# Optimization experiments

Hardware: AMD Instinct MI355X
Metric: run time of the kernel (lower is better)

## Reference

```python
import jax, jax.numpy as jnp
import numpy as np


def _gcn_conv(x, edge_index, W, b):
    # PyG GCNConv: h = x @ W; out = D^{-1/2}(A+I)D^{-1/2} h + b
    N = x.shape[0]
    src, dst = edge_index[0], edge_index[1]
    # degree with self-loops (edge weights = 1)
    deg = jax.ops.segment_sum(jnp.ones(src.shape[0], x.dtype), dst, num_segments=N) + 1.0
    dis = jax.lax.rsqrt(deg)  # deg >= 1 so finite
    h = x @ W  # [N, F_out]
    norm = dis[src] * dis[dst]  # [E]
    msg = h[src] * norm[:, None]  # [E, F_out] -- dominant memory traffic
    agg = jax.ops.segment_sum(msg, dst, num_segments=N)
    # self-loop contribution: norm_ii = dis_i^2
    out = agg + h * (dis * dis)[:, None] + b
    return out


def setup_inputs() -> dict:
    key = jax.random.key(0)
    k1, k2, k3, k4, k5, k6 = jax.random.split(key, 6)
    N, E = 100000, 1600000
    in_ch, hid, out_ch = 256, 128, 64  # hid = 2*out_channels
    x = jax.random.normal(k1, (N, in_ch), dtype=jnp.float32)
    edge_index = jax.random.randint(k2, (2, E), 0, N, dtype=jnp.int64)
    # Glorot-style init for GCN weights, zero bias (PyG default)
    W1 = jax.random.normal(k3, (in_ch, hid), dtype=jnp.float32) / np.sqrt(in_ch)
    b1 = jnp.zeros((hid,), jnp.float32)
    W2 = jax.random.normal(k4, (hid, out_ch), dtype=jnp.float32) / np.sqrt(hid)
    b2 = jnp.zeros((out_ch,), jnp.float32)
    return {"x": x, "edge_index": edge_index, "W1": W1, "b1": b1, "W2": W2, "b2": b2}


def reference(x, edge_index, W1, b1, W2, b2):
    # Encoder.forward: k=2 layers of activation(GCNConv(x, edge_index))
    h = jax.nn.relu(_gcn_conv(x, edge_index, W1, b1))
    h = jax.nn.relu(_gcn_conv(h, edge_index, W2, b2))
    return h
```

## Files before the change

kernel.cpp:

```cpp
#include <hip/hip_runtime.h>
#include <math.h>

#define THREADS 256

static inline int cdiv(long long a, long long b) { return (int)((a + b - 1) / b); }

typedef __attribute__((ext_vector_type(8))) short bf16x8;
typedef __attribute__((ext_vector_type(4))) float f32x4;

__device__ inline unsigned f2bf_rne_u(float f) {
    unsigned u = __builtin_bit_cast(unsigned, f);
    return (u + 0x7FFFu + ((u >> 16) & 1u)) >> 16;
}
__device__ inline float bfu2f(unsigned h) {
    unsigned u = h << 16;
    return __builtin_bit_cast(float, u);
}


__device__ __forceinline__ void hist_body(const int* __restrict__ dst, int* __restrict__ deg,
                                          int* __restrict__ rank, int E, int blk) {
    int base = (blk * THREADS + (int)threadIdx.x) * 4;
    if (base + 3 < E) {
        int4 d = *(const int4*)(dst + base);
        int4 r;
        r.x = atomicAdd(&deg[d.x], 1);
        r.y = atomicAdd(&deg[d.y], 1);
        r.z = atomicAdd(&deg[d.z], 1);
        r.w = atomicAdd(&deg[d.w], 1);
        *(int4*)(rank + base) = r;
    } else {
        for (int e = base; e < E; ++e) rank[e] = atomicAdd(&deg[dst[e]], 1);
    }
}

__device__ __forceinline__ void bfrag_unit(const float* __restrict__ W, short* __restrict__ frag,
                                           int NCT, int ctks, int lane) {
    int Nn = NCT * 16;
    int ct = ctks % NCT;
    int ks = ctks / NCT;
    int colc = ct * 16 + (lane & 15);
    int kbase = ks * 32 + (lane >> 4) * 8;
    short* base = frag + (size_t)ctks * 1024 + lane * 8;
    #pragma unroll
    for (int j = 0; j < 8; ++j) {
        float v = W[(size_t)(kbase + j) * Nn + colc];
        unsigned h = f2bf_rne_u(v);
        base[j] = (short)h;
        base[512 + j] = (short)f2bf_rne_u(v - bfu2f(h));
    }
}

__device__ __forceinline__ void fill_body(const int* __restrict__ src, const int* __restrict__ dst,
                                          const int* __restrict__ rank, const int* __restrict__ rowptr,
                                          int* __restrict__ col, int E, int blk) {
    int base = (blk * THREADS + (int)threadIdx.x) * 4;
    if (base + 3 < E) {
        int4 d = *(const int4*)(dst + base);
        int4 r = *(const int4*)(rank + base);
        int4 s = *(const int4*)(src + base);
        col[rowptr[d.x] + r.x] = s.x;
        col[rowptr[d.y] + r.y] = s.y;
        col[rowptr[d.z] + r.z] = s.z;
        col[rowptr[d.w] + r.w] = s.w;
    } else {
        for (int e = base; e < E; ++e)
            col[rowptr[dst[e]] + rank[e]] = src[e];
    }
}

template<int NCT, int KS>
__device__ __forceinline__ void gemm_body(const float* __restrict__ A, const short* __restrict__ Bfrag,
                                          unsigned short* __restrict__ G, const float* __restrict__ dis,
                                          int M, int blk) {
    constexpr int K = KS * 32;
    constexpr int Nn = NCT * 16;
    const int lane = threadIdx.x & 63;
    const int wave = threadIdx.x >> 6;
    const int rowBase = blk * 128 + wave * 32;
    const int arow0 = rowBase + (lane & 15);
    const int kgrp = (lane >> 4) * 8;

    f32x4 acc[2][NCT] = {};

    for (int ks = 0; ks < KS; ++ks) {
        const int kbase = ks * 32 + kgrp;
        bf16x8 ahi[2], alo[2];
        #pragma unroll
        for (int t = 0; t < 2; ++t) {
            int r = arow0 + t * 16;
            if (r >= M) r = M - 1;
            const float* ap = A + (size_t)r * K + kbase;
            float4 v0 = *(const float4*)ap;
            float4 v1 = *(const float4*)(ap + 4);
            float av[8] = {v0.x, v0.y, v0.z, v0.w, v1.x, v1.y, v1.z, v1.w};
            #pragma unroll
            for (int j = 0; j < 8; ++j) {
                unsigned h = f2bf_rne_u(av[j]);
                ahi[t][j] = (short)h;
                alo[t][j] = (short)f2bf_rne_u(av[j] - bfu2f(h));
            }
        }
        #pragma unroll
        for (int ct = 0; ct < NCT; ++ct) {
            const short* bp = Bfrag + (size_t)(ks * NCT + ct) * 1024 + lane * 8;
            bf16x8 bhi = *(const bf16x8*)bp;
            bf16x8 blo = *(const bf16x8*)(bp + 512);
            #pragma unroll
            for (int t = 0; t < 2; ++t) {
                acc[t][ct] = __builtin_amdgcn_mfma_f32_16x16x32_bf16(ahi[t], bhi, acc[t][ct], 0, 0, 0);
                acc[t][ct] = __builtin_amdgcn_mfma_f32_16x16x32_bf16(ahi[t], blo, acc[t][ct], 0, 0, 0);
                acc[t][ct] = __builtin_amdgcn_mfma_f32_16x16x32_bf16(alo[t], bhi, acc[t][ct], 0, 0, 0);
            }
        }
    }

    const int drow0 = rowBase + (lane >> 4) * 4;
    #pragma unroll
    for (int t = 0; t < 2; ++t) {
        #pragma unroll
        for (int r = 0; r < 4; ++r) {
            int row = drow0 + t * 16 + r;
            if (row < M) {
                float dval = dis[row];
                unsigned short* gp = G + (size_t)row * Nn + (lane & 15);
                #pragma unroll
                for (int ct = 0; ct < NCT; ++ct)
                    gp[ct * 16] = (unsigned short)f2bf_rne_u(acc[t][ct][r] * dval);
            }
        }
    }
}


__global__ __launch_bounds__(THREADS)
void hist_bfrag_kernel(const int* __restrict__ dst, int* __restrict__ deg, int* __restrict__ rank, int E,
                       const float* __restrict__ W1, short* __restrict__ bf1,
                       const float* __restrict__ W2, short* __restrict__ bf2, int nbHist) {
    int b = (int)blockIdx.x;
    if (b < nbHist) {
        hist_body(dst, deg, rank, E, b);
    } else {
        int u = (b - nbHist) * 4 + ((int)threadIdx.x >> 6);
        int lane = threadIdx.x & 63;
        if (u < 64) bfrag_unit(W1, bf1, 8, u, lane);
        else if (u < 80) bfrag_unit(W2, bf2, 4, u - 64, lane);
    }
}

template<int NCT, int KS>
__global__ __launch_bounds__(THREADS)
void fill_gemm_kernel(const int* __restrict__ src, const int* __restrict__ dst,
                      const int* __restrict__ rank, const int* __restrict__ rowptr,
                      int* __restrict__ col, int E,
                      const float* __restrict__ A, const short* __restrict__ Bfrag,
                      unsigned short* __restrict__ G, const float* __restrict__ dis,
                      int M, int nbFill) {
    int b = (int)blockIdx.x;
    if (b < nbFill) fill_body(src, dst, rank, rowptr, col, E, b);
    else gemm_body<NCT, KS>(A, Bfrag, G, dis, M, b - nbFill);
}

template<int NCT, int KS>
__global__ __launch_bounds__(THREADS)
void mfma_gemm_bf16out_kernel(const float* __restrict__ A, const short* __restrict__ Bfrag,
                              unsigned short* __restrict__ G, const float* __restrict__ dis,
                              int M) {
    gemm_body<NCT, KS>(A, Bfrag, G, dis, M, (int)blockIdx.x);
}


#define SCAN_BLOCK 256
#define SCAN_ITEMS 4

__global__ __launch_bounds__(SCAN_BLOCK)
void scan_block_kernel(const int* __restrict__ in, int* __restrict__ out,
                       int* __restrict__ blockSums, float* __restrict__ dis, int n) {
    __shared__ int sdata[SCAN_BLOCK];
    int base = blockIdx.x * (SCAN_BLOCK * SCAN_ITEMS);
    int tid = threadIdx.x;
    int v[SCAN_ITEMS];
    int sum = 0;
    #pragma unroll
    for (int k = 0; k < SCAN_ITEMS; ++k) {
        int idx = base + tid * SCAN_ITEMS + k;
        v[k] = (idx < n) ? in[idx] : 0;
        if (idx < n) dis[idx] = rsqrtf((float)v[k] + 1.0f);
        sum += v[k];
    }
    sdata[tid] = sum;
    __syncthreads();
    for (int off = 1; off < SCAN_BLOCK; off <<= 1) {
        int t = (tid >= off) ? sdata[tid - off] : 0;
        __syncthreads();
        sdata[tid] += t;
        __syncthreads();
    }
    if (tid == SCAN_BLOCK - 1) blockSums[blockIdx.x] = sdata[SCAN_BLOCK - 1];
    int run = (tid == 0) ? 0 : sdata[tid - 1];
    #pragma unroll
    for (int k = 0; k < SCAN_ITEMS; ++k) {
        int idx = base + tid * SCAN_ITEMS + k;
        if (idx < n) out[idx] = run;
        run += v[k];
    }
}

__global__ __launch_bounds__(SCAN_BLOCK)
void scan_sums_kernel(int* __restrict__ blockSums, int nB) {
    __shared__ int sdata[SCAN_BLOCK];
    int tid = threadIdx.x;
    sdata[tid] = (tid < nB) ? blockSums[tid] : 0;
    __syncthreads();
    for (int off = 1; off < SCAN_BLOCK; off <<= 1) {
        int t = (tid >= off) ? sdata[tid - off] : 0;
        __syncthreads();
        sdata[tid] += t;
        __syncthreads();
    }
    int excl = (tid == 0) ? 0 : sdata[tid - 1];
    if (tid < nB) blockSums[tid] = excl;
}

__global__ __launch_bounds__(SCAN_BLOCK)
void scan_add_kernel(int* __restrict__ out, const int* __restrict__ blockSums,
                     int n, int E) {
    int base = blockIdx.x * (SCAN_BLOCK * SCAN_ITEMS);
    int add = blockSums[blockIdx.x];
    #pragma unroll
    for (int k = 0; k < SCAN_ITEMS; ++k) {
        int idx = base + threadIdx.x * SCAN_ITEMS + k;
        if (idx < n) out[idx] += add;
    }
    if (blockIdx.x == 0 && threadIdx.x == 0) out[n] = E;
}


template<int F, int VEC>
__global__ __launch_bounds__(THREADS)
void gather_bf16_kernel(const unsigned short* __restrict__ g, const int* __restrict__ col,
                        const int* __restrict__ rowptr, const float* __restrict__ dis,
                        const float* __restrict__ bias, float* __restrict__ out, int N) {
    int wid = (int)((blockIdx.x * (long long)blockDim.x + threadIdx.x) >> 6);
    wid = __builtin_amdgcn_readfirstlane(wid);
    const int lane = threadIdx.x & 63;
    if (wid >= N) return;
    const float di = dis[wid];
    const int loff = lane * VEC;

    float acc0 = 0.0f, acc1 = 0.0f;

    auto loadrow = [&](int s) -> unsigned {
        const unsigned short* p = g + (size_t)s * F + loff;
        if (VEC == 2) return *(const unsigned*)p;
        else return (unsigned)*p;
    };
    auto addconv = [&](unsigned u) {
        if (VEC == 2) {
            acc0 += bfu2f(u & 0xFFFFu);
            acc1 += __builtin_bit_cast(float, u & 0xFFFF0000u);
        } else {
            acc0 += bfu2f(u);
        }
    };

    addconv(loadrow(wid));

    int start = __builtin_amdgcn_readfirstlane(rowptr[wid]);
    int end   = __builtin_amdgcn_readfirstlane(rowptr[wid + 1]);
    const int* c = col + start;
    int rem = end - start;

    if (rem >= 4) {
        int s0 = __builtin_amdgcn_readfirstlane(c[0]);
        int s1 = __builtin_amdgcn_readfirstlane(c[1]);
        int s2 = __builtin_amdgcn_readfirstlane(c[2]);
        int s3 = __builtin_amdgcn_readfirstlane(c[3]);
        unsigned u0 = loadrow(s0), u1 = loadrow(s1), u2 = loadrow(s2), u3 = loadrow(s3);
        c += 4; rem -= 4;
        while (rem >= 4) {
            int t0 = __builtin_amdgcn_readfirstlane(c[0]);
            int t1 = __builtin_amdgcn_readfirstlane(c[1]);
            int t2 = __builtin_amdgcn_readfirstlane(c[2]);
            int t3 = __builtin_amdgcn_readfirstlane(c[3]);
            unsigned v0 = loadrow(t0), v1 = loadrow(t1), v2 = loadrow(t2), v3 = loadrow(t3);
            addconv(u0); addconv(u1); addconv(u2); addconv(u3);
            u0 = v0; u1 = v1; u2 = v2; u3 = v3;
            c += 4; rem -= 4;
        }
        addconv(u0); addconv(u1); addconv(u2); addconv(u3);
    }
    while (rem > 0) {
        int s = __builtin_amdgcn_readfirstlane(c[0]);
        addconv(loadrow(s));
        ++c; --rem;
    }

    float* orow = out + (size_t)wid * F + loff;
    float v0 = di * acc0 + bias[loff];
    if (VEC == 2) {
        float v1 = di * acc1 + bias[loff + 1];
        float2 st = make_float2(fmaxf(v0, 0.0f), fmaxf(v1, 0.0f));
        *(float2*)orow = st;
    } else {
        *orow = fmaxf(v0, 0.0f);
    }
}


#define BM 64
#define BN 64
#define BK 16

__global__ __launch_bounds__(THREADS)
void sgemm_kernel(const float* __restrict__ A, const float* __restrict__ B,
                  float* __restrict__ C, int M, int N, int K) {
    __shared__ float As[BK][BM + 1];
    __shared__ float Bs[BK][BN + 1];

    const int tid = threadIdx.x;
    const int tr = tid / 16;
    const int tc = tid % 16;
    const int rowBase = blockIdx.y * BM;
    const int colBase = blockIdx.x * BN;

    float acc[4][4] = {};

    for (int k0 = 0; k0 < K; k0 += BK) {
        #pragma unroll
        for (int i = tid; i < BM * BK; i += THREADS) {
            int r = i / BK, c = i % BK;
            int gr = rowBase + r;
            As[c][r] = (gr < M) ? A[(size_t)gr * K + k0 + c] : 0.0f;
        }
        #pragma unroll
        for (int i = tid; i < BK * BN; i += THREADS) {
            int r = i / BN, c = i % BN;
            Bs[r][c] = B[(size_t)(k0 + r) * N + colBase + c];
        }
        __syncthreads();

        #pragma unroll
        for (int k = 0; k < BK; ++k) {
            float a[4], b[4];
            #pragma unroll
            for (int m = 0; m < 4; ++m) a[m] = As[k][tr * 4 + m];
            #pragma unroll
            for (int n = 0; n < 4; ++n) b[n] = Bs[k][tc * 4 + n];
            #pragma unroll
            for (int m = 0; m < 4; ++m)
                #pragma unroll
                for (int n = 0; n < 4; ++n)
                    acc[m][n] += a[m] * b[n];
        }
        __syncthreads();
    }

    #pragma unroll
    for (int m = 0; m < 4; ++m) {
        int gr = rowBase + tr * 4 + m;
        if (gr >= M) continue;
        #pragma unroll
        for (int n = 0; n < 4; ++n) {
            C[(size_t)gr * N + colBase + tc * 4 + n] = acc[m][n];
        }
    }
}

__global__ __launch_bounds__(THREADS)
void init_agg_kernel(const float* __restrict__ h, const float* __restrict__ dis,
                     float* __restrict__ agg, int N, int F) {
    int i = blockIdx.x * blockDim.x + threadIdx.x;
    int total = N * (F / 4);
    if (i >= total) return;
    int node = i / (F / 4);
    float d = dis[node];
    float w = d * d;
    float4 v = ((const float4*)h)[i];
    v.x *= w; v.y *= w; v.z *= w; v.w *= w;
    ((float4*)agg)[i] = v;
}

__global__ __launch_bounds__(THREADS)
void edge_scatter_kernel(const float* __restrict__ h, const int* __restrict__ src,
                         const int* __restrict__ dst, const float* __restrict__ dis,
                         float* __restrict__ agg, int E, int F) {
    int lanesPerEdge = F / 4;
    int tid = blockIdx.x * blockDim.x + threadIdx.x;
    int e = tid / lanesPerEdge;
    int c = tid % lanesPerEdge;
    if (e >= E) return;
    int s = src[e];
    int d = dst[e];
    float w = dis[s] * dis[d];
    float4 hv = ((const float4*)(h + (size_t)s * F))[c];
    float* ap = agg + (size_t)d * F + (size_t)c * 4;
    atomicAdd(ap + 0, hv.x * w);
    atomicAdd(ap + 1, hv.y * w);
    atomicAdd(ap + 2, hv.z * w);
    atomicAdd(ap + 3, hv.w * w);
}

__global__ __launch_bounds__(THREADS)
void finalize_kernel(const float* __restrict__ agg, const float* __restrict__ b,
                     float* __restrict__ out, int N, int F) {
    int i = blockIdx.x * blockDim.x + threadIdx.x;
    int total = N * (F / 4);
    if (i >= total) return;
    int c4 = i % (F / 4);
    float4 bv = ((const float4*)b)[c4];
    float4 v = ((const float4*)agg)[i];
    v.x = fmaxf(v.x + bv.x, 0.0f);
    v.y = fmaxf(v.y + bv.y, 0.0f);
    v.z = fmaxf(v.z + bv.z, 0.0f);
    v.w = fmaxf(v.w + bv.w, 0.0f);
    ((float4*)out)[i] = v;
}

__global__ __launch_bounds__(THREADS)
void fdeg_kernel(const int* __restrict__ dst, float* __restrict__ deg, int E) {
    int i = blockIdx.x * blockDim.x + threadIdx.x;
    if (i < E) atomicAdd(&deg[dst[i]], 1.0f);
}

__global__ __launch_bounds__(THREADS)
void fdis_kernel(float* __restrict__ deg, int N) {
    int i = blockIdx.x * blockDim.x + threadIdx.x;
    if (i < N) deg[i] = rsqrtf(deg[i] + 1.0f);
}


extern "C" void kernel_launch(void* const* d_in, const int* in_sizes, int n_in,
                              void* d_out, int out_size, void* d_ws, size_t ws_size,
                              hipStream_t stream) {
    const float* x  = (const float*)d_in[0];
    const int*   ei = (const int*)d_in[1];
    const float* W1 = (const float*)d_in[2];
    const float* b1 = (const float*)d_in[3];
    const float* W2 = (const float*)d_in[4];
    const float* b2 = (const float*)d_in[5];

    const int E    = in_sizes[1] / 2;
    const int hid  = in_sizes[3];
    const int outc = in_sizes[5];
    const int inc  = in_sizes[2] / hid;
    const int N    = in_sizes[0] / inc;

    const int* src = ei;
    const int* dst = ei + E;
    float* out = (float*)d_out;
    char* ws = (char*)d_ws;

    auto al = [](size_t v) { return (v + 255) & ~(size_t)255; };
    size_t o_dis  = 0;
    size_t o_deg  = al(o_dis + (size_t)N * 4);
    size_t o_rp   = al(o_deg + (size_t)N * 4);
    size_t o_bs   = al(o_rp + ((size_t)N + 1) * 4);
    size_t o_col  = al(o_bs + 4096);
    size_t o_rank = al(o_col + (size_t)E * 4);
    size_t o_bf1  = al(o_rank + (size_t)E * 4);
    size_t o_bf2  = al(o_bf1 + 131072);
    size_t o_G    = al(o_bf2 + 32768);
    size_t o_B    = al(o_G + (size_t)N * hid * 2);
    size_t need   = o_B + (size_t)N * hid * 4;

    if (ws_size >= need && N <= SCAN_BLOCK * SCAN_BLOCK * SCAN_ITEMS &&
        hid == 128 && outc == 64 && inc == 256) {
        float* dis    = (float*)(ws + o_dis);
        int*   deg    = (int*)(ws + o_deg);
        int*   rowptr = (int*)(ws + o_rp);
        int*   bsums  = (int*)(ws + o_bs);
        int*   col    = (int*)(ws + o_col);
        int*   rank   = (int*)(ws + o_rank);
        short* bf1    = (short*)(ws + o_bf1);
        short* bf2    = (short*)(ws + o_bf2);
        unsigned short* gbuf = (unsigned short*)(ws + o_G);
        float* out1   = (float*)(ws + o_B);

        const int nbHist = cdiv(E, 4 * THREADS);
        const int nbFill = cdiv(E, 4 * THREADS);
        const int nbGemm1 = cdiv(N, 128);

        hipMemsetAsync(deg, 0, (size_t)N * 4, stream);
        hist_bfrag_kernel<<<nbHist + 20, THREADS, 0, stream>>>(
            dst, deg, rank, E, W1, bf1, W2, bf2, nbHist);

        int nB = cdiv(N, SCAN_BLOCK * SCAN_ITEMS);
        scan_block_kernel<<<nB, SCAN_BLOCK, 0, stream>>>(deg, rowptr, bsums, dis, N);
        scan_sums_kernel<<<1, SCAN_BLOCK, 0, stream>>>(bsums, nB);
        scan_add_kernel<<<nB, SCAN_BLOCK, 0, stream>>>(rowptr, bsums, N, E);

        fill_gemm_kernel<8, 8><<<nbFill + nbGemm1, THREADS, 0, stream>>>(
            src, dst, rank, rowptr, col, E, x, bf1, gbuf, dis, N, nbFill);

        gather_bf16_kernel<128, 2><<<cdiv((long long)N * 64, THREADS), THREADS, 0, stream>>>(
            gbuf, col, rowptr, dis, b1, out1, N);

        mfma_gemm_bf16out_kernel<4, 4><<<cdiv(N, 128), THREADS, 0, stream>>>(out1, bf2, gbuf, dis, N);
        gather_bf16_kernel<64, 1><<<cdiv((long long)N * 64, THREADS), THREADS, 0, stream>>>(
            gbuf, col, rowptr, dis, b2, out, N);
        return;
    }

    float* dis = (float*)ws;
    size_t off1 = ((size_t)N * 4 + 255) & ~(size_t)255;
    float* h1 = (float*)(ws + off1);
    size_t off2 = off1 + ((((size_t)N * hid * 4) + 255) & ~(size_t)255);
    float* agg1 = (float*)(ws + off2);
    float* h2   = agg1;
    float* agg2 = agg1 + (size_t)N * outc;

    hipMemsetAsync(dis, 0, (size_t)N * 4, stream);
    fdeg_kernel<<<cdiv(E, THREADS), THREADS, 0, stream>>>(dst, dis, E);
    fdis_kernel<<<cdiv(N, THREADS), THREADS, 0, stream>>>(dis, N);

    {
        dim3 grid(hid / BN, cdiv(N, BM));
        sgemm_kernel<<<grid, THREADS, 0, stream>>>(x, W1, h1, N, hid, inc);
    }
    init_agg_kernel<<<cdiv((long long)N * hid / 4, THREADS), THREADS, 0, stream>>>(h1, dis, agg1, N, hid);
    edge_scatter_kernel<<<cdiv((long long)E * (hid / 4), THREADS), THREADS, 0, stream>>>(
        h1, src, dst, dis, agg1, E, hid);
    finalize_kernel<<<cdiv((long long)N * hid / 4, THREADS), THREADS, 0, stream>>>(agg1, b1, h1, N, hid);

    {
        dim3 grid(outc / BN, cdiv(N, BM));
        sgemm_kernel<<<grid, THREADS, 0, stream>>>(h1, W2, h2, N, outc, hid);
    }
    init_agg_kernel<<<cdiv((long long)N * outc / 4, THREADS), THREADS, 0, stream>>>(h2, dis, agg2, N, outc);
    edge_scatter_kernel<<<cdiv((long long)E * (outc / 4), THREADS), THREADS, 0, stream>>>(
        h2, src, dst, dis, agg2, E, outc);
    finalize_kernel<<<cdiv((long long)N * outc / 4, THREADS), THREADS, 0, stream>>>(agg2, b2, out, N, outc);
}
```

Before: 274.0 us.

## Co-schedule layer-1 GEMM with degree histogram and move source scaling into gather

Result: faster. 260.1 us (-5.1%).

```diff
diff --git a/kernel.cpp b/kernel.cpp
--- a/kernel.cpp
+++ b/kernel.cpp
@@ -18,17 +18,23 @@
 }
 
 
-__device__ __forceinline__ void hist_body(const int* __restrict__ dst, int* __restrict__ deg,
-                                          int* __restrict__ rank, int E, int blk) {
-    int base = (blk * THREADS + (int)threadIdx.x) * 4;
-    if (base + 3 < E) {
-        int4 d = *(const int4*)(dst + base);
-        int4 r;
-        r.x = atomicAdd(&deg[d.x], 1);
-        r.y = atomicAdd(&deg[d.y], 1);
-        r.z = atomicAdd(&deg[d.z], 1);
-        r.w = atomicAdd(&deg[d.w], 1);
-        *(int4*)(rank + base) = r;
+__device__ __forceinline__ void hist_body8(const int* __restrict__ dst, int* __restrict__ deg,
+                                           int* __restrict__ rank, int E, int blk) {
+    int base = (blk * THREADS + (int)threadIdx.x) * 8;
+    if (base + 7 < E) {
+        int4 d0 = *(const int4*)(dst + base);
+        int4 d1 = *(const int4*)(dst + base + 4);
+        int4 r0, r1;
+        r0.x = atomicAdd(&deg[d0.x], 1);
+        r0.y = atomicAdd(&deg[d0.y], 1);
+        r0.z = atomicAdd(&deg[d0.z], 1);
+        r0.w = atomicAdd(&deg[d0.w], 1);
+        r1.x = atomicAdd(&deg[d1.x], 1);
+        r1.y = atomicAdd(&deg[d1.y], 1);
+        r1.z = atomicAdd(&deg[d1.z], 1);
+        r1.w = atomicAdd(&deg[d1.w], 1);
+        *(int4*)(rank + base) = r0;
+        *(int4*)(rank + base + 4) = r1;
     } else {
         for (int e = base; e < E; ++e) rank[e] = atomicAdd(&deg[dst[e]], 1);
     }
@@ -71,8 +77,7 @@
 
 template<int NCT, int KS>
 __device__ __forceinline__ void gemm_body(const float* __restrict__ A, const short* __restrict__ Bfrag,
-                                          unsigned short* __restrict__ G, const float* __restrict__ dis,
-                                          int M, int blk) {
+                                          unsigned short* __restrict__ H, int M, int blk) {
     constexpr int K = KS * 32;
     constexpr int Nn = NCT * 16;
     const int lane = threadIdx.x & 63;
@@ -122,11 +127,10 @@
         for (int r = 0; r < 4; ++r) {
             int row = drow0 + t * 16 + r;
             if (row < M) {
-                float dval = dis[row];
-                unsigned short* gp = G + (size_t)row * Nn + (lane & 15);
+                unsigned short* hp = H + (size_t)row * Nn + (lane & 15);
                 #pragma unroll
                 for (int ct = 0; ct < NCT; ++ct)
-                    gp[ct * 16] = (unsigned short)f2bf_rne_u(acc[t][ct][r] * dval);
+                    hp[ct * 16] = (unsigned short)f2bf_rne_u(acc[t][ct][r]);
             }
         }
     }
@@ -134,39 +138,52 @@
 
 
 __global__ __launch_bounds__(THREADS)
-void hist_bfrag_kernel(const int* __restrict__ dst, int* __restrict__ deg, int* __restrict__ rank, int E,
+void zero_bfrag_kernel(int* __restrict__ deg, int N,
                        const float* __restrict__ W1, short* __restrict__ bf1,
-                       const float* __restrict__ W2, short* __restrict__ bf2, int nbHist) {
+                       const float* __restrict__ W2, short* __restrict__ bf2, int nbZero) {
     int b = (int)blockIdx.x;
-    if (b < nbHist) {
-        hist_body(dst, deg, rank, E, b);
+    if (b < nbZero) {
+        int base = (b * THREADS + (int)threadIdx.x) * 4;
+        if (base + 3 < N) {
+            *(int4*)(deg + base) = make_int4(0, 0, 0, 0);
+        } else {
+            for (int i = base; i < N; ++i) deg[i] = 0;
+        }
     } else {
-        int u = (b - nbHist) * 4 + ((int)threadIdx.x >> 6);
+        int u = (b - nbZero) * 4 + ((int)threadIdx.x >> 6);
         int lane = threadIdx.x & 63;
         if (u < 64) bfrag_unit(W1, bf1, 8, u, lane);
         else if (u < 80) bfrag_unit(W2, bf2, 4, u - 64, lane);
     }
 }
 
+__global__ __launch_bounds__(THREADS)
+void hist_gemm1_kernel(const int* __restrict__ dst, int* __restrict__ deg,
+                       int* __restrict__ rank, int E,
+                       const float* __restrict__ A, const short* __restrict__ Bfrag,
+                       unsigned short* __restrict__ H, int M,
+                       int nbHist, int nbGemm) {
+    int b = (int)blockIdx.x;
+    int total = nbHist + nbGemm;
+    long long t = (long long)b * nbGemm;
+    int gBefore = (int)(t / total);
+    bool isG = (((long long)(b + 1) * nbGemm) / total) > gBefore;
+    if (isG) gemm_body<8, 8>(A, Bfrag, H, M, gBefore);
+    else     hist_body8(dst, deg, rank, E, b - gBefore);
+}
+
+__global__ __launch_bounds__(THREADS)
+void fill_col_rank_kernel(const int* __restrict__ src, const int* __restrict__ dst,
+                          const int* __restrict__ rank, const int* __restrict__ rowptr,
+                          int* __restrict__ col, int E) {
+    fill_body(src, dst, rank, rowptr, col, E, (int)blockIdx.x);
+}
+
 template<int NCT, int KS>
 __global__ __launch_bounds__(THREADS)
-void fill_gemm_kernel(const int* __restrict__ src, const int* __restrict__ dst,
-                      const int* __restrict__ rank, const int* __restrict__ rowptr,
-                      int* __restrict__ col, int E,
-                      const float* __restrict__ A, const short* __restrict__ Bfrag,
-                      unsigned short* __restrict__ G, const float* __restrict__ dis,
-                      int M, int nbFill) {
-    int b = (int)blockIdx.x;
-    if (b < nbFill) fill_body(src, dst, rank, rowptr, col, E, b);
-    else gemm_body<NCT, KS>(A, Bfrag, G, dis, M, b - nbFill);
-}
-
-template<int NCT, int KS>
-__global__ __launch_bounds__(THREADS)
 void mfma_gemm_bf16out_kernel(const float* __restrict__ A, const short* __restrict__ Bfrag,
-                              unsigned short* __restrict__ G, const float* __restrict__ dis,
-                              int M) {
-    gemm_body<NCT, KS>(A, Bfrag, G, dis, M, (int)blockIdx.x);
+                              unsigned short* __restrict__ H, int M) {
+    gemm_body<NCT, KS>(A, Bfrag, H, M, (int)blockIdx.x);
 }
 
 
@@ -255,16 +272,16 @@
         if (VEC == 2) return *(const unsigned*)p;
         else return (unsigned)*p;
     };
-    auto addconv = [&](unsigned u) {
+    auto addconv = [&](unsigned u, float w) {
         if (VEC == 2) {
-            acc0 += bfu2f(u & 0xFFFFu);
-            acc1 += __builtin_bit_cast(float, u & 0xFFFF0000u);
+            acc0 += w * bfu2f(u & 0xFFFFu);
+            acc1 += w * __builtin_bit_cast(float, u & 0xFFFF0000u);
         } else {
-            acc0 += bfu2f(u);
+            acc0 += w * bfu2f(u);
         }
     };
 
-    addconv(loadrow(wid));
+    addconv(loadrow(wid), di);
 
     int start = __builtin_amdgcn_readfirstlane(rowptr[wid]);
     int end   = __builtin_amdgcn_readfirstlane(rowptr[wid + 1]);
@@ -276,6 +293,7 @@
         int s1 = __builtin_amdgcn_readfirstlane(c[1]);
         int s2 = __builtin_amdgcn_readfirstlane(c[2]);
         int s3 = __builtin_amdgcn_readfirstlane(c[3]);
+        float w0 = dis[s0], w1 = dis[s1], w2 = dis[s2], w3 = dis[s3];
         unsigned u0 = loadrow(s0), u1 = loadrow(s1), u2 = loadrow(s2), u3 = loadrow(s3);
         c += 4; rem -= 4;
         while (rem >= 4) {
@@ -283,16 +301,18 @@
             int t1 = __builtin_amdgcn_readfirstlane(c[1]);
             int t2 = __builtin_amdgcn_readfirstlane(c[2]);
             int t3 = __builtin_amdgcn_readfirstlane(c[3]);
+            float x0 = dis[t0], x1 = dis[t1], x2 = dis[t2], x3 = dis[t3];
             unsigned v0 = loadrow(t0), v1 = loadrow(t1), v2 = loadrow(t2), v3 = loadrow(t3);
-            addconv(u0); addconv(u1); addconv(u2); addconv(u3);
+            addconv(u0, w0); addconv(u1, w1); addconv(u2, w2); addconv(u3, w3);
             u0 = v0; u1 = v1; u2 = v2; u3 = v3;
+            w0 = x0; w1 = x1; w2 = x2; w3 = x3;
             c += 4; rem -= 4;
         }
-        addconv(u0); addconv(u1); addconv(u2); addconv(u3);
+        addconv(u0, w0); addconv(u1, w1); addconv(u2, w2); addconv(u3, w3);
     }
     while (rem > 0) {
         int s = __builtin_amdgcn_readfirstlane(c[0]);
-        addconv(loadrow(s));
+        addconv(loadrow(s), dis[s]);
         ++c; --rem;
     }
 
@@ -477,26 +497,27 @@
         unsigned short* gbuf = (unsigned short*)(ws + o_G);
         float* out1   = (float*)(ws + o_B);
 
-        const int nbHist = cdiv(E, 4 * THREADS);
-        const int nbFill = cdiv(E, 4 * THREADS);
+        const int nbZero  = cdiv(N, 4 * THREADS);
+        const int nbHist  = cdiv(E, 8 * THREADS);
         const int nbGemm1 = cdiv(N, 128);
-
-        hipMemsetAsync(deg, 0, (size_t)N * 4, stream);
-        hist_bfrag_kernel<<<nbHist + 20, THREADS, 0, stream>>>(
-            dst, deg, rank, E, W1, bf1, W2, bf2, nbHist);
+        const int nbFill  = cdiv(E, 4 * THREADS);
+
+        zero_bfrag_kernel<<<nbZero + 20, THREADS, 0, stream>>>(deg, N, W1, bf1, W2, bf2, nbZero);
+
+        hist_gemm1_kernel<<<nbHist + nbGemm1, THREADS, 0, stream>>>(
+            dst, deg, rank, E, x, bf1, gbuf, N, nbHist, nbGemm1);
 
         int nB = cdiv(N, SCAN_BLOCK * SCAN_ITEMS);
         scan_block_kernel<<<nB, SCAN_BLOCK, 0, stream>>>(deg, rowptr, bsums, dis, N);
         scan_sums_kernel<<<1, SCAN_BLOCK, 0, stream>>>(bsums, nB);
         scan_add_kernel<<<nB, SCAN_BLOCK, 0, stream>>>(rowptr, bsums, N, E);
 
-        fill_gemm_kernel<8, 8><<<nbFill + nbGemm1, THREADS, 0, stream>>>(
-            src, dst, rank, rowptr, col, E, x, bf1, gbuf, dis, N, nbFill);
+        fill_col_rank_kernel<<<nbFill, THREADS, 0, stream>>>(src, dst, rank, rowptr, col, E);
 
         gather_bf16_kernel<128, 2><<<cdiv((long long)N * 64, THREADS), THREADS, 0, stream>>>(
             gbuf, col, rowptr, dis, b1, out1, N);
 
-        mfma_gemm_bf16out_kernel<4, 4><<<cdiv(N, 128), THREADS, 0, stream>>>(out1, bf2, gbuf, dis, N);
+        mfma_gemm_bf16out_kernel<4, 4><<<cdiv(N, 128), THREADS, 0, stream>>>(out1, bf2, gbuf, N);
         gather_bf16_kernel<64, 1><<<cdiv((long long)N * 64, THREADS), THREADS, 0, stream>>>(
             gbuf, col, rowptr, dis, b2, out, N);
         return;
```
